# Kernel optimization log

Hardware: AMD Instinct MI355X
Metric: run time of the kernel (lower is better)

## Reference

```python
import jax, jax.numpy as jnp
import numpy as np

N_NODES = 100000
N_EDGES = 3200000
IN_CH = 128
HID_CH = 128   # 2 * out_channels
OUT_CH = 64


def setup_inputs() -> dict:
    key = jax.random.key(0)
    ks = jax.random.split(key, 6)
    x = jax.random.normal(ks[0], (N_NODES, IN_CH), dtype=jnp.float32)
    edge_index = jax.random.randint(ks[1], (2, N_EDGES), 0, N_NODES, dtype=jnp.int64)
    # Glorot-ish init for GCN linear weights
    W1 = jax.random.normal(ks[2], (IN_CH, HID_CH), dtype=jnp.float32) / np.sqrt(IN_CH)
    b1 = jnp.zeros((HID_CH,), dtype=jnp.float32)
    W2 = jax.random.normal(ks[3], (HID_CH, OUT_CH), dtype=jnp.float32) / np.sqrt(HID_CH)
    b2 = jnp.zeros((OUT_CH,), dtype=jnp.float32)
    return {"x": x, "edge_index": edge_index, "W1": W1, "b1": b1, "W2": W2, "b2": b2}


def gcn_conv(x, src, dst, W, b, n):
    """PyG GCNConv: add self-loops, symmetric D^-1/2 (A+I) D^-1/2 normalization,
    linear transform, scatter-add aggregation, then bias."""
    h = x @ W  # [N, C_out]
    ones = jnp.ones(src.shape[0], dtype=x.dtype)
    deg = jax.ops.segment_sum(ones, dst, num_segments=n) + 1.0  # self-loop degree
    dinv = jax.lax.rsqrt(deg)  # [N]
    coef = dinv[src] * dinv[dst]  # [E] edge normalization
    agg = jax.ops.segment_sum(h[src] * coef[:, None], dst, num_segments=n)
    agg = agg + h * (dinv * dinv)[:, None]  # self-loop contribution
    return agg + b


def reference(x, edge_index, W1, b1, W2, b2):
    src, dst = edge_index[0], edge_index[1]
    n = x.shape[0]
    h = jax.nn.relu(gcn_conv(x, src, dst, W1, b1, n))
    out = jax.nn.relu(gcn_conv(h, src, dst, W2, b2, n))
    return out
```

## Files before the change

kernel.cpp:

```cpp
#include <hip/hip_runtime.h>
#include <hip/hip_fp16.h>
#include <cstdint>
#include <cstddef>


#define BSHIFT 8
#define CAP    12288

typedef _Float16 half8 __attribute__((ext_vector_type(8)));
typedef float f32x4 __attribute__((ext_vector_type(4)));

__global__ __launch_bounds__(256) void k_binit(int* __restrict__ bktcur, int nbkt) {
  int b = blockIdx.x * 256 + threadIdx.x;
  if (b < nbkt) bktcur[b] = b * CAP;
}

__global__ __launch_bounds__(256) void k_part(const int* __restrict__ src,
                                              const int* __restrict__ dst,
                                              int* __restrict__ bktcur,
                                              int* __restrict__ part, int E,
                                              int nbkt) {
  __shared__ int hist[512];
  const int tid = threadIdx.x;
  const int e0 = blockIdx.x * 4096;
  for (int b = tid; b < nbkt; b += 256) hist[b] = 0;
  __syncthreads();
#pragma unroll
  for (int j = 0; j < 16; ++j) {
    const int e = e0 + j * 256 + tid;
    if (e < E) atomicAdd(&hist[dst[e] >> BSHIFT], 1);
  }
  __syncthreads();
  for (int b = tid; b < nbkt; b += 256) {
    const int c = hist[b];
    hist[b] = c ? atomicAdd(&bktcur[b], c) : 0;
  }
  __syncthreads();
#pragma unroll
  for (int j = 0; j < 16; ++j) {
    const int e = e0 + j * 256 + tid;
    if (e < E) {
      const int d = dst[e];
      const int bkt = d >> BSHIFT;
      const int pos = atomicAdd(&hist[bkt], 1);
      if (pos < (bkt + 1) * CAP)
        part[pos] = (src[e] << BSHIFT) | (d & ((1 << BSHIFT) - 1));
    }
  }
}

__global__ __launch_bounds__(256) void k_bktscan(const int* __restrict__ bktcur,
                                                 int* __restrict__ bktbase,
                                                 int* __restrict__ offsets, int n,
                                                 int E, int nbkt) {
  __shared__ int sc[512];
  const int t = threadIdx.x;
  sc[t] = (t < nbkt) ? (bktcur[t] - t * CAP) : 0;
  sc[256 + t] = (256 + t < nbkt) ? (bktcur[256 + t] - (256 + t) * CAP) : 0;
  __syncthreads();
  if (t == 0) {
    int run = 0;
    for (int b = 0; b < nbkt; ++b) {
      const int c = sc[b];
      sc[b] = run;
      run += c;
    }
    offsets[n] = E;
    bktbase[nbkt] = E;
  }
  __syncthreads();
  if (t < nbkt) bktbase[t] = sc[t];
  if (256 + t < nbkt) bktbase[256 + t] = sc[256 + t];
}

__global__ __launch_bounds__(256) void k_csr2(const int* __restrict__ part,
                                              const int* __restrict__ bktcur,
                                              const int* __restrict__ bktbase,
                                              int* __restrict__ offsets,
                                              int* __restrict__ csr_src,
                                              float* __restrict__ dinv, int n) {
  __shared__ int cnt[256];
  __shared__ int ts[256];
  const int b = blockIdx.x;
  const int node0 = b << BSHIFT;
  const int nn = min(256, n - node0);
  const int t = threadIdx.x;
  cnt[t] = 0;
  __syncthreads();
  const int w0p = b * CAP;
  const int w1p = min(bktcur[b], w0p + CAP);
  for (int e = w0p + t; e < w1p; e += 256)
    atomicAdd(&cnt[part[e] & ((1 << BSHIFT) - 1)], 1);
  __syncthreads();
  const int c = cnt[t];
  ts[t] = c;
  __syncthreads();
  for (int off = 1; off < 256; off <<= 1) {
    const int u = (t >= off) ? ts[t - off] : 0;
    __syncthreads();
    ts[t] += u;
    __syncthreads();
  }
  const int excl = ts[t] - c;
  const int w0 = bktbase[b];
  if (t < nn) {
    offsets[node0 + t] = w0 + excl;
    dinv[node0 + t] = rsqrtf((float)c + 1.0f);
  }
  cnt[t] = w0 + excl;
  __syncthreads();
  for (int e = w0p + t; e < w1p; e += 256) {
    const int p = part[e];
    const int pos = atomicAdd(&cnt[p & ((1 << BSHIFT) - 1)], 1);
    csr_src[pos] = p >> BSHIFT;
  }
}

template <typename TA, int COLS>
__global__ __launch_bounds__(256) void k_gemm_mfma(const TA* __restrict__ A,
                                                   const float* __restrict__ W,
                                                   __half* __restrict__ Hout,
                                                   int N, int ntiles) {
  constexpr int RW = (COLS == 128) ? 2 : 4;
  constexpr int RPT = RW * 16;
  __shared__ _Float16 Wt[128 * COLS];
  __shared__ _Float16 Lb[4][16][72];
  const int tid = threadIdx.x;
  const int w = tid >> 6;
  const int l = tid & 63;

  for (int f = tid; f < (128 * COLS) / 4; f += 256) {
    const int k = f / (COLS / 4);
    const int c4 = (f % (COLS / 4)) * 4;
    const float4 wv = *reinterpret_cast<const float4*>(W + (size_t)k * COLS + c4);
#pragma unroll
    for (int j = 0; j < 4; ++j) {
      const int cc = c4 + j;
      Wt[(cc * 128 + k) ^ ((cc & 7) << 3)] = (_Float16)(&wv.x)[j];
    }
  }
  __syncthreads();

  const int colw = (COLS == 128) ? (w >> 1) * 64 : 0;
  const int rw = (COLS == 128) ? (w & 1) : w;
  const int koff = (l >> 4) * 8;

  half8 bf[4][4];
#pragma unroll
  for (int t = 0; t < 4; ++t)
#pragma unroll
    for (int s = 0; s < 4; ++s) {
      const int cc = colw + 16 * t + (l & 15);
      const int kk = 32 * s + koff;
      bf[t][s] =
          *reinterpret_cast<const half8*>(&Wt[(cc * 128 + kk) ^ ((cc & 7) << 3)]);
    }

  for (int tile = blockIdx.x; tile < ntiles; tile += gridDim.x) {
    const int row = tile * RPT + rw * 16 + (l & 15);
    const int rowc = (row < N) ? row : (N - 1);
    f32x4 acc[4];
#pragma unroll
    for (int t = 0; t < 4; ++t) acc[t] = (f32x4){0.f, 0.f, 0.f, 0.f};

#pragma unroll
    for (int s = 0; s < 4; ++s) {
      half8 af;
      if constexpr (sizeof(TA) == 4) {
        const float* ap = (const float*)A + (size_t)rowc * 128 + 32 * s + koff;
        const float4 a0 = *reinterpret_cast<const float4*>(ap);
        const float4 a1 = *reinterpret_cast<const float4*>(ap + 4);
#pragma unroll
        for (int j = 0; j < 4; ++j) {
          af[j] = (_Float16)(&a0.x)[j];
          af[4 + j] = (_Float16)(&a1.x)[j];
        }
      } else {
        af = *reinterpret_cast<const half8*>((const __half*)A +
                                             (size_t)rowc * 128 + 32 * s + koff);
      }
#pragma unroll
      for (int t = 0; t < 4; ++t)
        acc[t] = __builtin_amdgcn_mfma_f32_16x16x32_f16(af, bf[t][s], acc[t],
                                                        0, 0, 0);
    }

#pragma unroll
    for (int t = 0; t < 4; ++t)
#pragma unroll
      for (int r = 0; r < 4; ++r)
        Lb[w][(l >> 4) * 4 + r][16 * t + (l & 15)] = (_Float16)acc[t][r];
    const int orow = tile * RPT + rw * 16 + (l & 15);
    if (orow < N) {
      const int ch = (l >> 4) * 16;
      const half8 v0 = *reinterpret_cast<const half8*>(&Lb[w][l & 15][ch]);
      const half8 v1 = *reinterpret_cast<const half8*>(&Lb[w][l & 15][ch + 8]);
      __half* hp = Hout + (size_t)orow * COLS + colw + ch;
      *reinterpret_cast<half8*>(hp) = v0;
      *reinterpret_cast<half8*>(hp + 8) = v1;
    }
  }
}

__global__ __launch_bounds__(256) void k_gather128(
    const __half* __restrict__ H, const int* __restrict__ offsets,
    const int* __restrict__ csr_src, const float* __restrict__ dinv,
    const float* __restrict__ bias, __half* __restrict__ out, int N) {
  const int lane = threadIdx.x & 63;
  const int g = lane >> 3;
  const int sl = lane & 7;
  int w = (blockIdx.x * 256 + threadIdx.x) >> 6;
  const int nw = (gridDim.x * 256) >> 6;
  for (int i = w; i < N; i += nw) {
    const float di = dinv[i];
    const int beg = offsets[i];
    const int end = offsets[i + 1];
    float acc[16];
    {
      const float cfs = (g == 0) ? di * di : 0.f;
      const float4 ha = *reinterpret_cast<const float4*>(H + (size_t)i * 128 + sl * 16);
      const float4 hb = *reinterpret_cast<const float4*>(H + (size_t)i * 128 + sl * 16 + 8);
      const __half2* hpa = reinterpret_cast<const __half2*>(&ha);
      const __half2* hpb = reinterpret_cast<const __half2*>(&hb);
#pragma unroll
      for (int q = 0; q < 4; ++q) {
        const float2 fa = __half22float2(hpa[q]);
        const float2 fb = __half22float2(hpb[q]);
        acc[q * 2] = cfs * fa.x;
        acc[q * 2 + 1] = cfs * fa.y;
        acc[8 + q * 2] = cfs * fb.x;
        acc[8 + q * 2 + 1] = cfs * fb.y;
      }
    }
    for (int base = beg; base < end; base += 8) {
      const int e = base + g;
      const bool v = e < end;
      const int s = v ? __builtin_nontemporal_load(csr_src + e) : i;
      const float cf = v ? dinv[s] * di : 0.f;
      const float4 ha = *reinterpret_cast<const float4*>(H + (size_t)s * 128 + sl * 16);
      const float4 hb = *reinterpret_cast<const float4*>(H + (size_t)s * 128 + sl * 16 + 8);
      const __half2* hpa = reinterpret_cast<const __half2*>(&ha);
      const __half2* hpb = reinterpret_cast<const __half2*>(&hb);
#pragma unroll
      for (int q = 0; q < 4; ++q) {
        const float2 fa = __half22float2(hpa[q]);
        const float2 fb = __half22float2(hpb[q]);
        acc[q * 2] = fmaf(cf, fa.x, acc[q * 2]);
        acc[q * 2 + 1] = fmaf(cf, fa.y, acc[q * 2 + 1]);
        acc[8 + q * 2] = fmaf(cf, fb.x, acc[8 + q * 2]);
        acc[8 + q * 2 + 1] = fmaf(cf, fb.y, acc[8 + q * 2 + 1]);
      }
    }
#pragma unroll
    for (int j = 0; j < 16; ++j) {
      float a = acc[j];
      a += __shfl_xor(a, 8);
      a += __shfl_xor(a, 16);
      a += __shfl_xor(a, 32);
      acc[j] = a;
    }
    if (g == 0) {
      __half2 ov[8];
#pragma unroll
      for (int q = 0; q < 8; ++q) {
        const float2 bv = *reinterpret_cast<const float2*>(bias + sl * 16 + q * 2);
        ov[q] = __floats2half2_rn(fmaxf(acc[q * 2] + bv.x, 0.f),
                                  fmaxf(acc[q * 2 + 1] + bv.y, 0.f));
      }
      __half* op = out + (size_t)i * 128 + sl * 16;
      *reinterpret_cast<float4*>(op) = *reinterpret_cast<const float4*>(&ov[0]);
      *reinterpret_cast<float4*>(op + 8) = *reinterpret_cast<const float4*>(&ov[4]);
    }
  }
}

__global__ __launch_bounds__(256) void k_gather64(
    const __half* __restrict__ H, const int* __restrict__ offsets,
    const int* __restrict__ csr_src, const float* __restrict__ dinv,
    const float* __restrict__ bias, float* __restrict__ out, int N) {
  const int lane = threadIdx.x & 63;
  const int g = lane >> 3;
  const int sl = lane & 7;
  int w = (blockIdx.x * 256 + threadIdx.x) >> 6;
  const int nw = (gridDim.x * 256) >> 6;
  for (int i = w; i < N; i += nw) {
    const float di = dinv[i];
    const int beg = offsets[i];
    const int end = offsets[i + 1];
    float acc[8];
    {
      const float cfs = (g == 0) ? di * di : 0.f;
      const float4 ha = *reinterpret_cast<const float4*>(H + (size_t)i * 64 + sl * 8);
      const __half2* hpa = reinterpret_cast<const __half2*>(&ha);
#pragma unroll
      for (int q = 0; q < 4; ++q) {
        const float2 fa = __half22float2(hpa[q]);
        acc[q * 2] = cfs * fa.x;
        acc[q * 2 + 1] = cfs * fa.y;
      }
    }
    for (int base = beg; base < end; base += 8) {
      const int e = base + g;
      const bool v = e < end;
      const int s = v ? __builtin_nontemporal_load(csr_src + e) : i;
      const float cf = v ? dinv[s] * di : 0.f;
      const float4 ha = *reinterpret_cast<const float4*>(H + (size_t)s * 64 + sl * 8);
      const __half2* hpa = reinterpret_cast<const __half2*>(&ha);
#pragma unroll
      for (int q = 0; q < 4; ++q) {
        const float2 fa = __half22float2(hpa[q]);
        acc[q * 2] = fmaf(cf, fa.x, acc[q * 2]);
        acc[q * 2 + 1] = fmaf(cf, fa.y, acc[q * 2 + 1]);
      }
    }
#pragma unroll
    for (int j = 0; j < 8; ++j) {
      float a = acc[j];
      a += __shfl_xor(a, 8);
      a += __shfl_xor(a, 16);
      a += __shfl_xor(a, 32);
      acc[j] = a;
    }
    if (g == 0) {
      float* op = out + (size_t)i * 64 + sl * 8;
      const float4 b0 = *reinterpret_cast<const float4*>(bias + sl * 8);
      const float4 b1 = *reinterpret_cast<const float4*>(bias + sl * 8 + 4);
      float4 o;
      o.x = fmaxf(acc[0] + b0.x, 0.f);
      o.y = fmaxf(acc[1] + b0.y, 0.f);
      o.z = fmaxf(acc[2] + b0.z, 0.f);
      o.w = fmaxf(acc[3] + b0.w, 0.f);
      *reinterpret_cast<float4*>(op) = o;
      o.x = fmaxf(acc[4] + b1.x, 0.f);
      o.y = fmaxf(acc[5] + b1.y, 0.f);
      o.z = fmaxf(acc[6] + b1.z, 0.f);
      o.w = fmaxf(acc[7] + b1.w, 0.f);
      *reinterpret_cast<float4*>(op + 4) = o;
    }
  }
}

extern "C" void kernel_launch(void* const* d_in, const int* in_sizes, int n_in,
                              void* d_out, int out_size, void* d_ws,
                              size_t ws_size, hipStream_t stream) {
  const float* x  = (const float*)d_in[0];
  const int*   ei = (const int*)d_in[1];
  const float* W1 = (const float*)d_in[2];
  const float* b1 = (const float*)d_in[3];
  const float* W2 = (const float*)d_in[4];
  const float* b2 = (const float*)d_in[5];

  const int IN  = 128;
  const int n   = in_sizes[0] / IN;
  const int E   = in_sizes[1] / 2;
  const int* srcv = ei;
  const int* dstv = ei + E;
  float* out = (float*)d_out;

  const int NBKT = (n + 255) >> BSHIFT;
  const int NCHK = (E + 4095) / 4096;
  const int NT1  = (n + 31) / 32;
  const int NT2  = (n + 63) / 64;

  char* p = (char*)d_ws;
  auto take = [&](size_t bytes) {
    char* r = p;
    p += (bytes + 255) & ~(size_t)255;
    return r;
  };
  float*  dinv    = (float*)take((size_t)n * 4);
  int*    offsets = (int*)take((size_t)(n + 1) * 4);
  int*    bktbase = (int*)take(512 * 4);
  int*    bktcur  = (int*)take(512 * 4);
  int*    csr_src = (int*)take((size_t)E * 4);
  __half* H16     = (__half*)take((size_t)n * 128 * 2);
  __half* hprime  = (__half*)take((size_t)n * 128 * 2);
  int*    part    = (int*)hprime;

  k_binit<<<(NBKT + 255) / 256, 256, 0, stream>>>(bktcur, NBKT);
  k_part<<<NCHK, 256, 0, stream>>>(srcv, dstv, bktcur, part, E, NBKT);
  k_bktscan<<<1, 256, 0, stream>>>(bktcur, bktbase, offsets, n, E, NBKT);
  k_csr2<<<NBKT, 256, 0, stream>>>(part, bktcur, bktbase, offsets, csr_src,
                                   dinv, n);

  k_gemm_mfma<float, 128><<<512, 256, 0, stream>>>(x, W1, H16, n, NT1);
  k_gather128<<<25000, 256, 0, stream>>>(H16, offsets, csr_src, dinv, b1,
                                         hprime, n);

  k_gemm_mfma<__half, 64><<<512, 256, 0, stream>>>(hprime, W2, H16, n, NT2);
  k_gather64<<<25000, 256, 0, stream>>>(H16, offsets, csr_src, dinv, b2,
                                        out, n);
}
```

Baseline: 356.0 us.

## Fold source dinv scaling into GEMM epilogue and unroll gather by two edges

The GEMM epilogue now multiplies each output row by dinv[row], so the gather kernels sum pre-scaled neighbour rows. The destination dinv is applied once per node at the end. This removes the per-edge random dinv[s] load and multiply from the gather loop. The gather main loop also processes 16 edges per iteration with two independent row loads per lane, for more memory-level parallelism, with an 8-wide tail loop for the remainder.

```diff
diff --git a/kernel.cpp b/kernel.cpp
--- a/kernel.cpp
+++ b/kernel.cpp
@@ -119,6 +119,7 @@
 template <typename TA, int COLS>
 __global__ __launch_bounds__(256) void k_gemm_mfma(const TA* __restrict__ A,
                                                    const float* __restrict__ W,
+                                                   const float* __restrict__ dinv,
                                                    __half* __restrict__ Hout,
                                                    int N, int ntiles) {
   constexpr int RW = (COLS == 128) ? 2 : 4;
@@ -185,11 +186,19 @@
                                                         0, 0, 0);
     }
 
+    const int rbase = tile * RPT + rw * 16 + (l >> 4) * 4;
+    float dr[4];
+#pragma unroll
+    for (int r = 0; r < 4; ++r) {
+      const int rr = rbase + r;
+      dr[r] = (rr < N) ? dinv[rr] : 0.f;
+    }
+
 #pragma unroll
     for (int t = 0; t < 4; ++t)
 #pragma unroll
       for (int r = 0; r < 4; ++r)
-        Lb[w][(l >> 4) * 4 + r][16 * t + (l & 15)] = (_Float16)acc[t][r];
+        Lb[w][(l >> 4) * 4 + r][16 * t + (l & 15)] = (_Float16)(acc[t][r] * dr[r]);
     const int orow = tile * RPT + rw * 16 + (l & 15);
     if (orow < N) {
       const int ch = (l >> 4) * 16;
@@ -212,43 +221,66 @@
   int w = (blockIdx.x * 256 + threadIdx.x) >> 6;
   const int nw = (gridDim.x * 256) >> 6;
   for (int i = w; i < N; i += nw) {
-    const float di = dinv[i];
     const int beg = offsets[i];
     const int end = offsets[i + 1];
     float acc[16];
     {
-      const float cfs = (g == 0) ? di * di : 0.f;
+      const float vf = (g == 0) ? 1.f : 0.f;
       const float4 ha = *reinterpret_cast<const float4*>(H + (size_t)i * 128 + sl * 16);
       const float4 hb = *reinterpret_cast<const float4*>(H + (size_t)i * 128 + sl * 16 + 8);
-      const __half2* hpa = reinterpret_cast<const __half2*>(&ha);
-      const __half2* hpb = reinterpret_cast<const __half2*>(&hb);
-#pragma unroll
-      for (int q = 0; q < 4; ++q) {
-        const float2 fa = __half22float2(hpa[q]);
-        const float2 fb = __half22float2(hpb[q]);
-        acc[q * 2] = cfs * fa.x;
-        acc[q * 2 + 1] = cfs * fa.y;
-        acc[8 + q * 2] = cfs * fb.x;
-        acc[8 + q * 2 + 1] = cfs * fb.y;
-      }
-    }
-    for (int base = beg; base < end; base += 8) {
+      const __half2* pa = reinterpret_cast<const __half2*>(&ha);
+      const __half2* pb = reinterpret_cast<const __half2*>(&hb);
+#pragma unroll
+      for (int q = 0; q < 4; ++q) {
+        const float2 fa = __half22float2(pa[q]);
+        const float2 fb = __half22float2(pb[q]);
+        acc[q * 2] = vf * fa.x;
+        acc[q * 2 + 1] = vf * fa.y;
+        acc[8 + q * 2] = vf * fb.x;
+        acc[8 + q * 2 + 1] = vf * fb.y;
+      }
+    }
+    int base = beg;
+    for (; base + 16 <= end; base += 16) {
+      const int s0 = __builtin_nontemporal_load(csr_src + base + g);
+      const int s1 = __builtin_nontemporal_load(csr_src + base + 8 + g);
+      const float4 h0a = *reinterpret_cast<const float4*>(H + (size_t)s0 * 128 + sl * 16);
+      const float4 h0b = *reinterpret_cast<const float4*>(H + (size_t)s0 * 128 + sl * 16 + 8);
+      const float4 h1a = *reinterpret_cast<const float4*>(H + (size_t)s1 * 128 + sl * 16);
+      const float4 h1b = *reinterpret_cast<const float4*>(H + (size_t)s1 * 128 + sl * 16 + 8);
+      const __half2* p0a = reinterpret_cast<const __half2*>(&h0a);
+      const __half2* p0b = reinterpret_cast<const __half2*>(&h0b);
+      const __half2* p1a = reinterpret_cast<const __half2*>(&h1a);
+      const __half2* p1b = reinterpret_cast<const __half2*>(&h1b);
+#pragma unroll
+      for (int q = 0; q < 4; ++q) {
+        const float2 f0a = __half22float2(p0a[q]);
+        const float2 f0b = __half22float2(p0b[q]);
+        const float2 f1a = __half22float2(p1a[q]);
+        const float2 f1b = __half22float2(p1b[q]);
+        acc[q * 2] += f0a.x + f1a.x;
+        acc[q * 2 + 1] += f0a.y + f1a.y;
+        acc[8 + q * 2] += f0b.x + f1b.x;
+        acc[8 + q * 2 + 1] += f0b.y + f1b.y;
+      }
+    }
+    for (; base < end; base += 8) {
       const int e = base + g;
       const bool v = e < end;
       const int s = v ? __builtin_nontemporal_load(csr_src + e) : i;
-      const float cf = v ? dinv[s] * di : 0.f;
+      const float vf = v ? 1.f : 0.f;
       const float4 ha = *reinterpret_cast<const float4*>(H + (size_t)s * 128 + sl * 16);
       const float4 hb = *reinterpret_cast<const float4*>(H + (size_t)s * 128 + sl * 16 + 8);
-      const __half2* hpa = reinterpret_cast<const __half2*>(&ha);
-      const __half2* hpb = reinterpret_cast<const __half2*>(&hb);
-#pragma unroll
-      for (int q = 0; q < 4; ++q) {
-        const float2 fa = __half22float2(hpa[q]);
-        const float2 fb = __half22float2(hpb[q]);
-        acc[q * 2] = fmaf(cf, fa.x, acc[q * 2]);
-        acc[q * 2 + 1] = fmaf(cf, fa.y, acc[q * 2 + 1]);
-        acc[8 + q * 2] = fmaf(cf, fb.x, acc[8 + q * 2]);
-        acc[8 + q * 2 + 1] = fmaf(cf, fb.y, acc[8 + q * 2 + 1]);
+      const __half2* pa = reinterpret_cast<const __half2*>(&ha);
+      const __half2* pb = reinterpret_cast<const __half2*>(&hb);
+#pragma unroll
+      for (int q = 0; q < 4; ++q) {
+        const float2 fa = __half22float2(pa[q]);
+        const float2 fb = __half22float2(pb[q]);
+        acc[q * 2] = fmaf(vf, fa.x, acc[q * 2]);
+        acc[q * 2 + 1] = fmaf(vf, fa.y, acc[q * 2 + 1]);
+        acc[8 + q * 2] = fmaf(vf, fb.x, acc[8 + q * 2]);
+        acc[8 + q * 2 + 1] = fmaf(vf, fb.y, acc[8 + q * 2 + 1]);
       }
     }
 #pragma unroll
@@ -260,12 +292,13 @@
       acc[j] = a;
     }
     if (g == 0) {
+      const float di = dinv[i];
       __half2 ov[8];
 #pragma unroll
       for (int q = 0; q < 8; ++q) {
         const float2 bv = *reinterpret_cast<const float2*>(bias + sl * 16 + q * 2);
-        ov[q] = __floats2half2_rn(fmaxf(acc[q * 2] + bv.x, 0.f),
-                                  fmaxf(acc[q * 2 + 1] + bv.y, 0.f));
+        ov[q] = __floats2half2_rn(fmaxf(fmaf(di, acc[q * 2], bv.x), 0.f),
+                                  fmaxf(fmaf(di, acc[q * 2 + 1], bv.y), 0.f));
       }
       __half* op = out + (size_t)i * 128 + sl * 16;
       *reinterpret_cast<float4*>(op) = *reinterpret_cast<const float4*>(&ov[0]);
@@ -284,33 +317,48 @@
   int w = (blockIdx.x * 256 + threadIdx.x) >> 6;
   const int nw = (gridDim.x * 256) >> 6;
   for (int i = w; i < N; i += nw) {
-    const float di = dinv[i];
     const int beg = offsets[i];
     const int end = offsets[i + 1];
     float acc[8];
     {
-      const float cfs = (g == 0) ? di * di : 0.f;
+      const float vf = (g == 0) ? 1.f : 0.f;
       const float4 ha = *reinterpret_cast<const float4*>(H + (size_t)i * 64 + sl * 8);
-      const __half2* hpa = reinterpret_cast<const __half2*>(&ha);
-#pragma unroll
-      for (int q = 0; q < 4; ++q) {
-        const float2 fa = __half22float2(hpa[q]);
-        acc[q * 2] = cfs * fa.x;
-        acc[q * 2 + 1] = cfs * fa.y;
-      }
-    }
-    for (int base = beg; base < end; base += 8) {
+      const __half2* pa = reinterpret_cast<const __half2*>(&ha);
+#pragma unroll
+      for (int q = 0; q < 4; ++q) {
+        const float2 fa = __half22float2(pa[q]);
+        acc[q * 2] = vf * fa.x;
+        acc[q * 2 + 1] = vf * fa.y;
+      }
+    }
+    int base = beg;
+    for (; base + 16 <= end; base += 16) {
+      const int s0 = __builtin_nontemporal_load(csr_src + base + g);
+      const int s1 = __builtin_nontemporal_load(csr_src + base + 8 + g);
+      const float4 h0 = *reinterpret_cast<const float4*>(H + (size_t)s0 * 64 + sl * 8);
+      const float4 h1 = *reinterpret_cast<const float4*>(H + (size_t)s1 * 64 + sl * 8);
+      const __half2* p0 = reinterpret_cast<const __half2*>(&h0);
+      const __half2* p1 = reinterpret_cast<const __half2*>(&h1);
+#pragma unroll
+      for (int q = 0; q < 4; ++q) {
+        const float2 f0 = __half22float2(p0[q]);
+        const float2 f1 = __half22float2(p1[q]);
+        acc[q * 2] += f0.x + f1.x;
+        acc[q * 2 + 1] += f0.y + f1.y;
+      }
+    }
+    for (; base < end; base += 8) {
       const int e = base + g;
       const bool v = e < end;
       const int s = v ? __builtin_nontemporal_load(csr_src + e) : i;
-      const float cf = v ? dinv[s] * di : 0.f;
+      const float vf = v ? 1.f : 0.f;
       const float4 ha = *reinterpret_cast<const float4*>(H + (size_t)s * 64 + sl * 8);
-      const __half2* hpa = reinterpret_cast<const __half2*>(&ha);
-#pragma unroll
-      for (int q = 0; q < 4; ++q) {
-        const float2 fa = __half22float2(hpa[q]);
-        acc[q * 2] = fmaf(cf, fa.x, acc[q * 2]);
-        acc[q * 2 + 1] = fmaf(cf, fa.y, acc[q * 2 + 1]);
+      const __half2* pa = reinterpret_cast<const __half2*>(&ha);
+#pragma unroll
+      for (int q = 0; q < 4; ++q) {
+        const float2 fa = __half22float2(pa[q]);
+        acc[q * 2] = fmaf(vf, fa.x, acc[q * 2]);
+        acc[q * 2 + 1] = fmaf(vf, fa.y, acc[q * 2 + 1]);
       }
     }
 #pragma unroll
@@ -322,19 +370,20 @@
       acc[j] = a;
     }
     if (g == 0) {
+      const float di = dinv[i];
       float* op = out + (size_t)i * 64 + sl * 8;
       const float4 b0 = *reinterpret_cast<const float4*>(bias + sl * 8);
       const float4 b1 = *reinterpret_cast<const float4*>(bias + sl * 8 + 4);
       float4 o;
-      o.x = fmaxf(acc[0] + b0.x, 0.f);
-      o.y = fmaxf(acc[1] + b0.y, 0.f);
-      o.z = fmaxf(acc[2] + b0.z, 0.f);
-      o.w = fmaxf(acc[3] + b0.w, 0.f);
+      o.x = fmaxf(fmaf(di, acc[0], b0.x), 0.f);
+      o.y = fmaxf(fmaf(di, acc[1], b0.y), 0.f);
+      o.z = fmaxf(fmaf(di, acc[2], b0.z), 0.f);
+      o.w = fmaxf(fmaf(di, acc[3], b0.w), 0.f);
       *reinterpret_cast<float4*>(op) = o;
-      o.x = fmaxf(acc[4] + b1.x, 0.f);
-      o.y = fmaxf(acc[5] + b1.y, 0.f);
-      o.z = fmaxf(acc[6] + b1.z, 0.f);
-      o.w = fmaxf(acc[7] + b1.w, 0.f);
+      o.x = fmaxf(fmaf(di, acc[4], b1.x), 0.f);
+      o.y = fmaxf(fmaf(di, acc[5], b1.y), 0.f);
+      o.z = fmaxf(fmaf(di, acc[6], b1.z), 0.f);
+      o.w = fmaxf(fmaf(di, acc[7], b1.w), 0.f);
       *reinterpret_cast<float4*>(op + 4) = o;
     }
   }
@@ -383,11 +432,11 @@
   k_csr2<<<NBKT, 256, 0, stream>>>(part, bktcur, bktbase, offsets, csr_src,
                                    dinv, n);
 
-  k_gemm_mfma<float, 128><<<512, 256, 0, stream>>>(x, W1, H16, n, NT1);
+  k_gemm_mfma<float, 128><<<512, 256, 0, stream>>>(x, W1, dinv, H16, n, NT1);
   k_gather128<<<25000, 256, 0, stream>>>(H16, offsets, csr_src, dinv, b1,
                                          hprime, n);
 
-  k_gemm_mfma<__half, 64><<<512, 256, 0, stream>>>(hprime, W2, H16, n, NT2);
+  k_gemm_mfma<__half, 64><<<512, 256, 0, stream>>>(hprime, W2, dinv, H16, n, NT2);
   k_gather64<<<25000, 256, 0, stream>>>(H16, offsets, csr_src, dinv, b2,
                                         out, n);
 }
```

Result: faster. 316.0 us (-11.3%).
